# Kernel optimization log

Hardware: AMD Instinct MI355X
Metric: run time of the kernel (lower is better)

Reference implementation:

```python
import jax, jax.numpy as jnp
import numpy as np

B, N, C, H = 32, 577, 768, 12  # seq len = num_patches + 1 (cls token)
HD = C // H
SCALE = HD ** -0.5


def setup_inputs() -> dict:
    key = jax.random.key(0)
    k1, k2, k3, k4, k5 = jax.random.split(key, 5)
    x = jax.random.normal(k1, (B, N, C), dtype=jnp.float32)
    qkv_w = jax.random.normal(k2, (3 * C, C), dtype=jnp.float32) * (C ** -0.5)
    proj_w = jax.random.normal(k3, (C, C), dtype=jnp.float32) * (C ** -0.5)
    proj_b = jax.random.normal(k4, (C,), dtype=jnp.float32) * 0.02
    # learned additive distance-bias mask (nn.Parameter in the original)
    attn_mask = jax.random.normal(k5, (H, N, N), dtype=jnp.float32) * 0.02
    return {"x": x, "qkv_w": qkv_w, "proj_w": proj_w, "proj_b": proj_b,
            "attn_mask": attn_mask}


def reference(x, qkv_w, proj_w, proj_b, attn_mask):
    b, n, c = x.shape
    # fused QKV projection (no bias, qkv_bias=False)
    qkv = (x @ qkv_w.T).reshape(b, n, 3, H, HD)
    qkv = jnp.transpose(qkv, (2, 0, 3, 1, 4))  # [3, B, H, N, HD]
    q, k, v = qkv[0], qkv[1], qkv[2]
    # scaled dot-product scores + learned additive mask (broadcast over batch)
    attn = jnp.einsum('bhnd,bhmd->bhnm', q, k) * SCALE + attn_mask
    attn = jax.nn.softmax(attn, axis=-1)
    out = jnp.einsum('bhnm,bhmd->bhnd', attn, v)
    out = jnp.transpose(out, (0, 2, 1, 3)).reshape(b, n, c)
    return out @ proj_w.T + proj_b
```

## Files before the change

kernel.cpp:

```cpp
#include <hip/hip_runtime.h>
#include <stdint.h>
#include <stddef.h>

#define B_SZ 32
#define NQ 577
#define CDIM 768
#define NH 12
#define HDIM 64
#define MROWS (B_SZ * NQ)
#define KDIM CDIM
#define NKT (KDIM / 64)
#define VT_STRIDE 640
#define MK_STRIDE 640
#define SCALE_F 0.125f

typedef __bf16 bf16x8 __attribute__((ext_vector_type(8)));
typedef float f32x4 __attribute__((ext_vector_type(4)));
typedef unsigned short u16x8 __attribute__((ext_vector_type(8)));
typedef unsigned short u16x4 __attribute__((ext_vector_type(4)));

__device__ __forceinline__ unsigned short f2bf(float f) {
    unsigned int u = __builtin_bit_cast(unsigned int, f);
    return (unsigned short)((u + 0x7fffu + ((u >> 16) & 1u)) >> 16);
}
__device__ __forceinline__ float bf2f(unsigned short u) {
    unsigned int v = ((unsigned int)u) << 16;
    return __builtin_bit_cast(float, v);
}

__device__ __forceinline__ f32x4 mfma16(bf16x8 a, bf16x8 b, f32x4 c) {
    return __builtin_amdgcn_mfma_f32_16x16x32_bf16(a, b, c, 0, 0, 0);
}

__device__ __forceinline__ void gll16(const void* g, void* l) {
    __builtin_amdgcn_global_load_lds(
        (const __attribute__((address_space(1))) void*)g,
        (__attribute__((address_space(3))) void*)l, 16, 0, 0);
}

__global__ __launch_bounds__(256) void cvt_bf16(
    const float* __restrict__ src, unsigned short* __restrict__ dst, int n8)
{
    int i = blockIdx.x * blockDim.x + threadIdx.x;
    int stride = gridDim.x * blockDim.x;
    for (; i < n8; i += stride) {
        const float* p = src + (size_t)i * 8;
        f32x4 v0 = *(const f32x4*)p;
        f32x4 v1 = *(const f32x4*)(p + 4);
        u16x8 u;
        u[0] = f2bf(v0[0]); u[1] = f2bf(v0[1]); u[2] = f2bf(v0[2]); u[3] = f2bf(v0[3]);
        u[4] = f2bf(v1[0]); u[5] = f2bf(v1[1]); u[6] = f2bf(v1[2]); u[7] = f2bf(v1[3]);
        *(u16x8*)(dst + (size_t)i * 8) = u;
    }
}

__global__ __launch_bounds__(256) void cvt_mask(
    const float* __restrict__ src, unsigned short* __restrict__ dst)
{
    const int CH = MK_STRIDE / 8;
    int i = blockIdx.x * blockDim.x + threadIdx.x;
    int total = NH * NQ * CH;
    if (i >= total) return;
    int row = i / CH, c8 = (i % CH) * 8;
    const float* s = src + (size_t)row * NQ;
    u16x8 u;
#pragma unroll
    for (int j = 0; j < 8; ++j) {
        int c = c8 + j;
        u[j] = (c < NQ) ? f2bf(s[c]) : (unsigned short)0;
    }
    *(u16x8*)(dst + (size_t)row * MK_STRIDE + c8) = u;
}


#define STAGE_HT8(SC, A_PTR, B_PTR)                                                \
    { const int _t = (SC) >> 2, _p = (SC) & 3;                                     \
      if (_t < NKT) {                                                              \
        const int _kh = _p >> 1;                                                   \
        unsigned short* _dst = (_p & 1) ? &Bl[_t & 1][_kh][0] : &Al[_t & 1][_kh][0];\
        const unsigned short* _sb = (_p & 1) ? (B_PTR) : (A_PTR);                  \
        const int _rb = ((_p & 1) ? nt : mt) * 256;                                \
        const int _k = _t * 64 + _kh * 32;                                         \
        const int _c0 = tid, _c1 = tid + 512;                                      \
        const int _g0 = _c0 ^ ((_c0 >> 3) & 7), _g1 = _c1 ^ ((_c1 >> 3) & 7);      \
        int _r0 = _rb + (_g0 >> 2), _r1 = _rb + (_g1 >> 2);                        \
        if (!(_p & 1)) {                                                           \
            if (_r0 >= MROWS) _r0 = MROWS - 1;                                     \
            if (_r1 >= MROWS) _r1 = MROWS - 1;                                     \
        }                                                                          \
        gll16(_sb + (size_t)_r0 * KDIM + _k + (_g0 & 3) * 8, _dst + _c0 * 8);      \
        gll16(_sb + (size_t)_r1 * KDIM + _k + (_g1 & 3) * 8, _dst + _c1 * 8);      \
      } else {                                                                     \
        gll16(A_PTR, &Scr[tid * 8]);                                               \
        gll16(A_PTR, &Scr[(tid + 512) * 8]);                                       \
      } }

#define GEMM8_MAINLOOP(A_PTR, B_PTR)                                               \
    const int tid = threadIdx.x;                                                   \
    const int wid = tid >> 6, lane = tid & 63;                                     \
    const int lo = lane & 15, hi = lane >> 4;                                      \
    const int wr = wid >> 2, wcN = wid & 3;                                        \
    f32x4 acc[8][4];                                                               \
    _Pragma("unroll") for (int i = 0; i < 8; ++i)                                  \
        _Pragma("unroll") for (int j = 0; j < 4; ++j)                              \
            acc[i][j] = (f32x4){0.f, 0.f, 0.f, 0.f};                               \
    const int xsw = ((4 * lo + hi) ^ ((lo >> 1) & 7)) * 16;                        \
    _Pragma("unroll") for (int ps = 0; ps < 7; ++ps) { STAGE_HT8(ps, A_PTR, B_PTR) } \
    int sc = 7;                                                                    \
    asm volatile("s_waitcnt vmcnt(6)" ::: "memory");                               \
    __builtin_amdgcn_s_barrier();                                                  \
    for (int t = 0; t < NKT; ++t) {                                                \
        const int db = t & 1;                                                      \
        const char* a0p = (const char*)&Al[db][0][0] + xsw;                        \
        const char* a1p = (const char*)&Al[db][1][0] + xsw;                        \
        const char* b0p = (const char*)&Bl[db][0][0] + xsw;                        \
        const char* b1p = (const char*)&Bl[db][1][0] + xsw;                        \
        bf16x8 a[8], bx[2], by[2];                                                 \
              \
        _Pragma("unroll") for (int mi = 0; mi < 8; ++mi)                           \
            a[mi] = *(const bf16x8*)(a0p + (wr * 8 + mi) * 1024);                  \
        bx[0] = *(const bf16x8*)(b0p + (wcN * 4 + 0) * 1024);                      \
        bx[1] = *(const bf16x8*)(b0p + (wcN * 4 + 1) * 1024);                      \
        asm volatile("" ::: "memory");                                             \
        STAGE_HT8(sc, A_PTR, B_PTR) ++sc;                                          \
        __builtin_amdgcn_s_barrier();                                              \
        __builtin_amdgcn_s_setprio(1);                                             \
        _Pragma("unroll") for (int mi = 0; mi < 8; ++mi) {                         \
            acc[mi][0] = mfma16(a[mi], bx[0], acc[mi][0]);                         \
            acc[mi][1] = mfma16(a[mi], bx[1], acc[mi][1]);                         \
        }                                                                          \
        __builtin_amdgcn_s_setprio(0);                                             \
        __builtin_amdgcn_s_barrier();                                              \
                               \
        by[0] = *(const bf16x8*)(b0p + (wcN * 4 + 2) * 1024);                      \
        by[1] = *(const bf16x8*)(b0p + (wcN * 4 + 3) * 1024);                      \
        asm volatile("" ::: "memory");                                             \
        STAGE_HT8(sc, A_PTR, B_PTR) ++sc;                                          \
        __builtin_amdgcn_s_barrier();                                              \
        __builtin_amdgcn_s_setprio(1);                                             \
        _Pragma("unroll") for (int mi = 0; mi < 8; ++mi) {                         \
            acc[mi][2] = mfma16(a[mi], by[0], acc[mi][2]);                         \
            acc[mi][3] = mfma16(a[mi], by[1], acc[mi][3]);                         \
        }                                                                          \
        __builtin_amdgcn_s_setprio(0);                                             \
        __builtin_amdgcn_s_barrier();                                              \
                    \
        _Pragma("unroll") for (int mi = 0; mi < 8; ++mi)                           \
            a[mi] = *(const bf16x8*)(a1p + (wr * 8 + mi) * 1024);                  \
        bx[0] = *(const bf16x8*)(b1p + (wcN * 4 + 0) * 1024);                      \
        bx[1] = *(const bf16x8*)(b1p + (wcN * 4 + 1) * 1024);                      \
        asm volatile("" ::: "memory");                                             \
        STAGE_HT8(sc, A_PTR, B_PTR) ++sc;                                          \
        __builtin_amdgcn_s_barrier();                                              \
        __builtin_amdgcn_s_setprio(1);                                             \
        _Pragma("unroll") for (int mi = 0; mi < 8; ++mi) {                         \
            acc[mi][0] = mfma16(a[mi], bx[0], acc[mi][0]);                         \
            acc[mi][1] = mfma16(a[mi], bx[1], acc[mi][1]);                         \
        }                                                                          \
        __builtin_amdgcn_s_setprio(0);                                             \
        __builtin_amdgcn_s_barrier();                                              \
               \
        by[0] = *(const bf16x8*)(b1p + (wcN * 4 + 2) * 1024);                      \
        by[1] = *(const bf16x8*)(b1p + (wcN * 4 + 3) * 1024);                      \
        asm volatile("" ::: "memory");                                             \
        STAGE_HT8(sc, A_PTR, B_PTR) ++sc;                                          \
        asm volatile("s_waitcnt vmcnt(6)" ::: "memory");                           \
        __builtin_amdgcn_s_barrier();                                              \
        __builtin_amdgcn_s_setprio(1);                                             \
        _Pragma("unroll") for (int mi = 0; mi < 8; ++mi) {                         \
            acc[mi][2] = mfma16(a[mi], by[0], acc[mi][2]);                         \
            acc[mi][3] = mfma16(a[mi], by[1], acc[mi][3]);                         \
        }                                                                          \
        __builtin_amdgcn_s_setprio(0);                                             \
        __builtin_amdgcn_s_barrier();                                              \
    }                                                                              \
    asm volatile("s_waitcnt vmcnt(0)" ::: "memory");

__global__ __launch_bounds__(512, 2) void qkv_gemm(
    const unsigned short* __restrict__ A,
    const unsigned short* __restrict__ Bm,
    unsigned short* __restrict__ qb,
    unsigned short* __restrict__ kb,
    unsigned short* __restrict__ vtb)
{
    __shared__ __align__(16) unsigned short Al[2][2][256 * 32];
    __shared__ __align__(16) unsigned short Bl[2][2][256 * 32];
    __shared__ __align__(16) unsigned short Scr[512 * 16];
    const int NTL = 9;
    const int xcd = blockIdx.x & 7, off = blockIdx.x >> 3;
    const int wgid = (xcd < 1 ? xcd * 83 : 83 + (xcd - 1) * 82) + off;
    const int nt = wgid % NTL, mt = wgid / NTL;

    GEMM8_MAINLOOP(A, Bm)

    const int cbase = nt * 256 + wcN * 64;
    const int s = cbase / CDIM;
    const int h = (cbase % CDIM) / HDIM;
#pragma unroll
    for (int mi = 0; mi < 8; ++mi) {
#pragma unroll
        for (int r = 0; r < 4; ++r) {
            int m = mt * 256 + wr * 128 + mi * 16 + 4 * hi + r;
            if (m >= MROWS) continue;
            int b = m / NQ, n = m % NQ;
            size_t bh = (size_t)(b * NH + h);
#pragma unroll
            for (int nj = 0; nj < 4; ++nj) {
                int d = nj * 16 + lo;
                unsigned short bv = f2bf(acc[mi][nj][r]);
                if (s == 0)      qb[(bh * NQ + n) * HDIM + d] = bv;
                else if (s == 1) kb[(bh * NQ + n) * HDIM + d] = bv;
                else             vtb[(bh * HDIM + d) * VT_STRIDE + n] = bv;
            }
        }
    }
}

__global__ __launch_bounds__(512, 2) void proj_gemm(
    const unsigned short* __restrict__ A,
    const unsigned short* __restrict__ Bm,
    const float* __restrict__ bias,
    float* __restrict__ out)
{
    __shared__ __align__(16) unsigned short Al[2][2][256 * 32];
    __shared__ __align__(16) unsigned short Bl[2][2][256 * 32];
    __shared__ __align__(16) unsigned short Scr[512 * 16];
    const int NTL = 3;
    const int xcd = blockIdx.x & 7, off = blockIdx.x >> 3;
    const int wgid = (xcd < 3 ? xcd * 28 : 84 + (xcd - 3) * 27) + off;
    const int nt = wgid % NTL, mt = wgid / NTL;

    GEMM8_MAINLOOP(A, Bm)

    const int cb = nt * 256 + wcN * 64;
    float bv[4];
#pragma unroll
    for (int nj = 0; nj < 4; ++nj) bv[nj] = bias[cb + nj * 16 + lo];
#pragma unroll
    for (int mi = 0; mi < 8; ++mi) {
#pragma unroll
        for (int r = 0; r < 4; ++r) {
            int m = mt * 256 + wr * 128 + mi * 16 + 4 * hi + r;
            if (m >= MROWS) continue;
#pragma unroll
            for (int nj = 0; nj < 4; ++nj)
                out[(size_t)m * CDIM + cb + nj * 16 + lo] = acc[mi][nj][r] + bv[nj];
        }
    }
}

#define STAGE(SEL, KV)                                                        \
    {                                                                         \
        int kr0 = (KV) + srow;      if (kr0 > NQ - 1) kr0 = NQ - 1;           \
        int kr1 = (KV) + srow + 32; if (kr1 > NQ - 1) kr1 = NQ - 1;           \
        gll16(kp + (size_t)kr0 * HDIM + scol, &Ks[SEL][0] + tid * 8);         \
        gll16(kp + (size_t)kr1 * HDIM + scol, &Ks[SEL][2048] + tid * 8);      \
        gll16(vp + (size_t)srow * VT_STRIDE + (KV) + scol, &Vs[SEL][0] + tid * 8); \
        gll16(vp + (size_t)(srow + 32) * VT_STRIDE + (KV) + scol, &Vs[SEL][2048] + tid * 8); \
    }

#define LOADM(MW, KV)                                                         \
    _Pragma("unroll") for (int nj = 0; nj < 4; ++nj)                          \
        MW[nj] = *(const u16x4*)(mrow + (KV) + 16 * nj + 4 * hi);

#define ATTN_COMPUTE(CB, KV)                                                  \
    {                                                                         \
        const int kv0 = (KV);                                                 \
        bf16x8 af0[4], af1[4], bv0[4], bv1[4];                                \
        _Pragma("unroll") for (int nj = 0; nj < 4; ++nj) {                    \
            int kr = 16 * nj + lo;                                            \
            int sw = (kr & 7) << 4;                                           \
            const unsigned short* rowp = &Ks[CB][kr * 64];                    \
            af0[nj] = *(const bf16x8*)(rowp + ((( 0 + 16 * hi) ^ sw) >> 1));  \
            af1[nj] = *(const bf16x8*)(rowp + (((64 + 16 * hi) ^ sw) >> 1));  \
        }                                                                     \
        _Pragma("unroll") for (int dj = 0; dj < 4; ++dj) {                    \
            int dr = 16 * dj + lo;                                            \
            int sw = (dr & 7) << 4;                                           \
            const unsigned short* rowp = &Vs[CB][dr * 64];                    \
            bv0[dj] = *(const bf16x8*)(rowp + ((( 0 + 16 * hi) ^ sw) >> 1));  \
            bv1[dj] = *(const bf16x8*)(rowp + (((64 + 16 * hi) ^ sw) >> 1));  \
        }                                                                     \
        __builtin_amdgcn_s_setprio(1);                                        \
        f32x4 S[4];                                                           \
        _Pragma("unroll") for (int nj = 0; nj < 4; ++nj) {                    \
            f32x4 sv = (f32x4){0.f, 0.f, 0.f, 0.f};                           \
            sv = mfma16(af0[nj], bq0, sv);                                    \
            sv = mfma16(af1[nj], bq1, sv);                                    \
            S[nj] = sv;                                                       \
        }                                                                     \
        __builtin_amdgcn_s_setprio(0);                                        \
        float p[16];                                                          \
        _Pragma("unroll") for (int nj = 0; nj < 4; ++nj)                      \
            _Pragma("unroll") for (int r = 0; r < 4; ++r)                     \
                p[nj * 4 + r] = S[nj][r] * SCALE_F + bf2f(mw[nj][r]);         \
        if (kv0 + 64 > NQ) {                                                  \
            const int rem = NQ - kv0;                                         \
            _Pragma("unroll") for (int nj = 0; nj < 4; ++nj)                  \
                _Pragma("unroll") for (int r = 0; r < 4; ++r)                 \
                    if (16 * nj + 4 * hi + r >= rem) p[nj * 4 + r] = -1e30f;  \
        }                                                                     \
        float m01 = fmaxf(p[0], p[1]),  m23 = fmaxf(p[2], p[3]);              \
        float m45 = fmaxf(p[4], p[5]),  m67 = fmaxf(p[6], p[7]);              \
        float m89 = fmaxf(p[8], p[9]),  mab = fmaxf(p[10], p[11]);            \
        float mcd = fmaxf(p[12], p[13]), mef = fmaxf(p[14], p[15]);           \
        float pmax = fmaxf(fmaxf(fmaxf(m01, m23), fmaxf(m45, m67)),           \
                           fmaxf(fmaxf(m89, mab), fmaxf(mcd, mef)));          \
        pmax = fmaxf(pmax, __shfl_xor(pmax, 16));                             \
        pmax = fmaxf(pmax, __shfl_xor(pmax, 32));                             \
        bool grow = pmax > m_run + 8.f;                                       \
        float mnew = grow ? pmax : m_run;                                     \
        float corr = __expf(m_run - mnew);                                    \
        m_run = mnew;                                                         \
        if (__any((int)grow)) {                                               \
            float c0 = __shfl(corr, 4 * hi + 0);                              \
            float c1 = __shfl(corr, 4 * hi + 1);                              \
            float c2 = __shfl(corr, 4 * hi + 2);                              \
            float c3 = __shfl(corr, 4 * hi + 3);                              \
            _Pragma("unroll") for (int dj = 0; dj < 4; ++dj) {                \
                accO[dj][0] *= c0; accO[dj][1] *= c1;                         \
                accO[dj][2] *= c2; accO[dj][3] *= c3;                         \
            }                                                                 \
        }                                                                     \
        _Pragma("unroll") for (int i = 0; i < 16; ++i)                        \
            p[i] = __expf(p[i] - mnew);                                       \
        float ps = (((p[0]+p[1])+(p[2]+p[3])) + ((p[4]+p[5])+(p[6]+p[7])))    \
                 + (((p[8]+p[9])+(p[10]+p[11])) + ((p[12]+p[13])+(p[14]+p[15])));\
        _Pragma("unroll") for (int nj = 0; nj < 4; ++nj) {                    \
            u16x4 w;                                                          \
            w[0] = f2bf(p[nj*4+0]); w[1] = f2bf(p[nj*4+1]);                   \
            w[2] = f2bf(p[nj*4+2]); w[3] = f2bf(p[nj*4+3]);                   \
            *(u16x4*)&P_lds[wv][lo][16 * nj + 4 * hi] = w;                    \
        }                                                                     \
        ps += __shfl_xor(ps, 16);                                             \
        ps += __shfl_xor(ps, 32);                                             \
        l_run = l_run * corr + ps;                                            \
        const bf16x8 pa0 = *(const bf16x8*)&P_lds[wv][lo][8 * hi];            \
        const bf16x8 pa1 = *(const bf16x8*)&P_lds[wv][lo][32 + 8 * hi];       \
        __builtin_amdgcn_s_setprio(1);                                        \
        _Pragma("unroll") for (int dj = 0; dj < 4; ++dj) {                    \
            accO[dj] = mfma16(pa0, bv0[dj], accO[dj]);                        \
            accO[dj] = mfma16(pa1, bv1[dj], accO[dj]);                        \
        }                                                                     \
        __builtin_amdgcn_s_setprio(0);                                        \
    }

__global__ __launch_bounds__(256) void attn_fused(
    const unsigned short* __restrict__ qb,
    const unsigned short* __restrict__ kb,
    const unsigned short* __restrict__ vtb,
    const unsigned short* __restrict__ maskb,
    unsigned short* __restrict__ ob)
{
    __shared__ unsigned short Ks[2][64 * 64];
    __shared__ unsigned short Vs[2][64 * 64];
    __shared__ unsigned short P_lds[4][16][68];
    const int tid = threadIdx.x;
    const int wv = tid >> 6;
    const int lane = tid & 63;
    const int lo = lane & 15, hi = lane >> 4;

    const int xcd = blockIdx.x & 7;
    const int idx = blockIdx.x >> 3;
    const int bh = xcd + 8 * (idx / 10);
    const int qblk = idx % 10;
    const int b = bh / NH, h = bh % NH;
    const int qt0 = qblk * 64;

    const unsigned short* qp = qb + (size_t)bh * NQ * HDIM;
    const unsigned short* kp = kb + (size_t)bh * NQ * HDIM;
    const unsigned short* vp = vtb + (size_t)bh * HDIM * VT_STRIDE;

    const int srow = tid >> 3;
    const int scol = ((((tid & 7) << 4) ^ ((srow & 7) << 4)) >> 1);

    int qr = qt0 + 16 * wv + lo; if (qr > NQ - 1) qr = NQ - 1;
    const unsigned short* mrow = maskb + ((size_t)h * NQ + qr) * MK_STRIDE;
    const bf16x8 bq0 = *(const bf16x8*)(qp + (size_t)qr * HDIM + 8 * hi);
    const bf16x8 bq1 = *(const bf16x8*)(qp + (size_t)qr * HDIM + 32 + 8 * hi);

    float m_run = -1e30f, l_run = 0.f;
    f32x4 accO[4];
#pragma unroll
    for (int dj = 0; dj < 4; ++dj) accO[dj] = (f32x4){0.f, 0.f, 0.f, 0.f};

    u16x4 mw[4];
    STAGE(0, 0)
    for (int t = 0; t < 9; ++t) {
        const int kv0 = t * 64;
        LOADM(mw, kv0)
        asm volatile("" ::: "memory");
        STAGE((t + 1) & 1, kv0 + 64)
        asm volatile("s_waitcnt vmcnt(8)" ::: "memory");
        __builtin_amdgcn_s_barrier();
        asm volatile("" ::: "memory");
        ATTN_COMPUTE(t & 1, kv0)
        asm volatile("" ::: "memory");
        __builtin_amdgcn_s_barrier();
    }
    LOADM(mw, 576)
    asm volatile("s_waitcnt vmcnt(4)" ::: "memory");
    __builtin_amdgcn_s_barrier();
    asm volatile("" ::: "memory");
    ATTN_COMPUTE(1, 576)

    float linv[4];
#pragma unroll
    for (int r = 0; r < 4; ++r) linv[r] = 1.0f / __shfl(l_run, 4 * hi + r);
#pragma unroll
    for (int r = 0; r < 4; ++r) {
        int row = qt0 + 16 * wv + 4 * hi + r;
        if (row >= NQ) continue;
        size_t base = ((size_t)b * NQ + row) * CDIM + h * HDIM;
#pragma unroll
        for (int dj = 0; dj < 4; ++dj)
            ob[base + dj * 16 + lo] = f2bf(accO[dj][r] * linv[r]);
    }
}

extern "C" void kernel_launch(void* const* d_in, const int* in_sizes, int n_in,
                              void* d_out, int out_size, void* d_ws, size_t ws_size,
                              hipStream_t stream) {
    (void)in_sizes; (void)n_in; (void)out_size; (void)ws_size;
    const float* x      = (const float*)d_in[0];
    const float* qkv_w  = (const float*)d_in[1];
    const float* proj_w = (const float*)d_in[2];
    const float* proj_b = (const float*)d_in[3];
    const float* mask   = (const float*)d_in[4];
    float* out = (float*)d_out;

    const size_t x_elems  = (size_t)MROWS * CDIM;
    const size_t w_elems  = (size_t)3 * CDIM * CDIM;
    const size_t pw_elems = (size_t)CDIM * CDIM;
    const size_t mk_elems = (size_t)NH * NQ * MK_STRIDE;
    const size_t qk_elems = (size_t)B_SZ * NH * NQ * HDIM;
    const size_t vt_elems = (size_t)B_SZ * NH * HDIM * VT_STRIDE;

    unsigned short* xb    = (unsigned short*)d_ws;
    unsigned short* wb    = xb + x_elems;
    unsigned short* pwb   = wb + w_elems;
    unsigned short* mkb   = pwb + pw_elems;
    unsigned short* vtbuf = mkb + mk_elems;
    unsigned short* qbuf  = vtbuf + vt_elems;
    unsigned short* kbuf  = qbuf + qk_elems;
    unsigned short* aobuf = xb;

    cvt_bf16<<<1024, 256, 0, stream>>>(x, xb, (int)(x_elems / 8));
    cvt_bf16<<<256, 256, 0, stream>>>(qkv_w, wb, (int)(w_elems / 8));
    cvt_bf16<<<128, 256, 0, stream>>>(proj_w, pwb, (int)(pw_elems / 8));
    cvt_mask<<<(NH * NQ * (MK_STRIDE / 8) + 255) / 256, 256, 0, stream>>>(mask, mkb);
    qkv_gemm<<<73 * 9, 512, 0, stream>>>(xb, wb, qbuf, kbuf, vtbuf);
    attn_fused<<<12 * 32 * 10, 256, 0, stream>>>(qbuf, kbuf, vtbuf, mkb, aobuf);
    proj_gemm<<<73 * 3, 512, 0, stream>>>(aobuf, pwb, proj_b, out);
}
```

Measured before the change: 311.6 us.

## Replace QKV GEMM with simpler 128x128 tile kernel using 256 threads

The QKV projection moves from the heavily pipelined 256x256-tile, 512-thread kernel to a simpler 128x128-tile, 256-thread kernel. It uses double-buffered direct-to-LDS loads over 32-wide K steps, with its own XCD-aware block mapping over 2610 blocks. The aim is more blocks and better wave balance across CUs for this shape. In exchange it gives up the deeper software pipeline and the swizzled LDS layout, which may cost data reuse and add LDS bank conflicts.

```diff
diff --git a/kernel.cpp b/kernel.cpp
--- a/kernel.cpp
+++ b/kernel.cpp
@@ -72,6 +72,90 @@
     *(u16x8*)(dst + (size_t)row * MK_STRIDE + c8) = u;
 }
 
+#define GEMM_MAINLOOP(A_PTR, B_PTR, MCLAMP)                                        \
+    const int tid = threadIdx.x;                                                   \
+    const int wv = tid >> 6, lane = tid & 63;                                      \
+    const int lo = lane & 15, hi = lane >> 4;                                      \
+    const int wr = wv >> 1, wc = wv & 1;                                           \
+    f32x4 acc[4][4];                                                               \
+    _Pragma("unroll") for (int i = 0; i < 4; ++i)                                  \
+        _Pragma("unroll") for (int j = 0; j < 4; ++j)                              \
+            acc[i][j] = (f32x4){0.f, 0.f, 0.f, 0.f};                               \
+    const int c0 = wv * 128 + lane;                                                \
+    const int c1 = c0 + 64;                                                        \
+    const int rA0 = c0 >> 2, kA0 = (c0 & 3) * 8;                                   \
+    const int rA1 = c1 >> 2, kA1 = (c1 & 3) * 8;                                   \
+    int gra0 = mt * 128 + rA0; if (MCLAMP && gra0 >= MROWS) gra0 = MROWS - 1;      \
+    int gra1 = mt * 128 + rA1; if (MCLAMP && gra1 >= MROWS) gra1 = MROWS - 1;      \
+    const int grb0 = nt * 128 + rA0, grb1 = nt * 128 + rA1;                        \
+    gll16(A_PTR + (size_t)gra0 * KDIM + kA0, &As[0][c0 * 8]);                      \
+    gll16(A_PTR + (size_t)gra1 * KDIM + kA1, &As[0][c1 * 8]);                      \
+    gll16(B_PTR + (size_t)grb0 * KDIM + kA0, &Bs[0][c0 * 8]);                      \
+    gll16(B_PTR + (size_t)grb1 * KDIM + kA1, &Bs[0][c1 * 8]);                      \
+    for (int ks = 0; ks < KDIM / 32; ++ks) {                                       \
+        const int cur = ks & 1, nxt = cur ^ 1;                                     \
+        if (ks + 1 < KDIM / 32) {                                                  \
+            const int k0n = (ks + 1) * 32;                                         \
+            gll16(A_PTR + (size_t)gra0 * KDIM + k0n + kA0, &As[nxt][c0 * 8]);      \
+            gll16(A_PTR + (size_t)gra1 * KDIM + k0n + kA1, &As[nxt][c1 * 8]);      \
+            gll16(B_PTR + (size_t)grb0 * KDIM + k0n + kA0, &Bs[nxt][c0 * 8]);      \
+            gll16(B_PTR + (size_t)grb1 * KDIM + k0n + kA1, &Bs[nxt][c1 * 8]);      \
+            asm volatile("s_waitcnt vmcnt(4)" ::: "memory");                       \
+        } else {                                                                   \
+            asm volatile("s_waitcnt vmcnt(0)" ::: "memory");                       \
+        }                                                                          \
+        __builtin_amdgcn_s_barrier();                                              \
+        bf16x8 af[4], bfr[4];                                                      \
+        _Pragma("unroll") for (int mi = 0; mi < 4; ++mi)                           \
+            af[mi] = *(const bf16x8*)(&As[cur][(wr * 64 + mi * 16 + lo) * 32 + hi * 8]); \
+        _Pragma("unroll") for (int nj = 0; nj < 4; ++nj)                           \
+            bfr[nj] = *(const bf16x8*)(&Bs[cur][(wc * 64 + nj * 16 + lo) * 32 + hi * 8]); \
+        __builtin_amdgcn_s_setprio(1);                                             \
+        _Pragma("unroll") for (int mi = 0; mi < 4; ++mi)                           \
+            _Pragma("unroll") for (int nj = 0; nj < 4; ++nj)                       \
+                acc[mi][nj] = mfma16(af[mi], bfr[nj], acc[mi][nj]);                \
+        __builtin_amdgcn_s_setprio(0);                                             \
+        __builtin_amdgcn_s_barrier();                                              \
+    }
+
+__global__ __launch_bounds__(256) void qkv_gemm(
+    const unsigned short* __restrict__ A,
+    const unsigned short* __restrict__ Bm,
+    unsigned short* __restrict__ qb,
+    unsigned short* __restrict__ kb,
+    unsigned short* __restrict__ vtb)
+{
+    __shared__ unsigned short As[2][128 * 32];
+    __shared__ unsigned short Bs[2][128 * 32];
+    const int NT = 18;
+    const int q8 = 326, r8 = 2;
+    const int xcd = blockIdx.x & 7, off = blockIdx.x >> 3;
+    const int wgid = (xcd < r8 ? xcd * (q8 + 1) : r8 * (q8 + 1) + (xcd - r8) * q8) + off;
+    int nt = wgid % NT, mt = wgid / NT;
+
+    GEMM_MAINLOOP(A, Bm, 1)
+
+    const int s = nt / 6;
+    const int h = (nt % 6) * 2 + wc;
+#pragma unroll
+    for (int mi = 0; mi < 4; ++mi) {
+#pragma unroll
+        for (int r = 0; r < 4; ++r) {
+            int m = mt * 128 + wr * 64 + mi * 16 + hi * 4 + r;
+            if (m >= MROWS) continue;
+            int b = m / NQ, n = m % NQ;
+            size_t bh = (size_t)(b * NH + h);
+#pragma unroll
+            for (int nj = 0; nj < 4; ++nj) {
+                int d = nj * 16 + lo;
+                unsigned short bv = f2bf(acc[mi][nj][r]);
+                if (s == 0)      qb[(bh * NQ + n) * HDIM + d] = bv;
+                else if (s == 1) kb[(bh * NQ + n) * HDIM + d] = bv;
+                else             vtb[(bh * HDIM + d) * VT_STRIDE + n] = bv;
+            }
+        }
+    }
+}
 
 #define STAGE_HT8(SC, A_PTR, B_PTR)                                                \
     { const int _t = (SC) >> 2, _p = (SC) & 3;                                     \
@@ -116,7 +200,6 @@
         const char* b0p = (const char*)&Bl[db][0][0] + xsw;                        \
         const char* b1p = (const char*)&Bl[db][1][0] + xsw;                        \
         bf16x8 a[8], bx[2], by[2];                                                 \
-              \
         _Pragma("unroll") for (int mi = 0; mi < 8; ++mi)                           \
             a[mi] = *(const bf16x8*)(a0p + (wr * 8 + mi) * 1024);                  \
         bx[0] = *(const bf16x8*)(b0p + (wcN * 4 + 0) * 1024);                      \
@@ -131,7 +214,6 @@
         }                                                                          \
         __builtin_amdgcn_s_setprio(0);                                             \
         __builtin_amdgcn_s_barrier();                                              \
-                               \
         by[0] = *(const bf16x8*)(b0p + (wcN * 4 + 2) * 1024);                      \
         by[1] = *(const bf16x8*)(b0p + (wcN * 4 + 3) * 1024);                      \
         asm volatile("" ::: "memory");                                             \
@@ -144,7 +226,6 @@
         }                                                                          \
         __builtin_amdgcn_s_setprio(0);                                             \
         __builtin_amdgcn_s_barrier();                                              \
-                    \
         _Pragma("unroll") for (int mi = 0; mi < 8; ++mi)                           \
             a[mi] = *(const bf16x8*)(a1p + (wr * 8 + mi) * 1024);                  \
         bx[0] = *(const bf16x8*)(b1p + (wcN * 4 + 0) * 1024);                      \
@@ -159,7 +240,6 @@
         }                                                                          \
         __builtin_amdgcn_s_setprio(0);                                             \
         __builtin_amdgcn_s_barrier();                                              \
-               \
         by[0] = *(const bf16x8*)(b1p + (wcN * 4 + 2) * 1024);                      \
         by[1] = *(const bf16x8*)(b1p + (wcN * 4 + 3) * 1024);                      \
         asm volatile("" ::: "memory");                                             \
@@ -175,46 +255,6 @@
         __builtin_amdgcn_s_barrier();                                              \
     }                                                                              \
     asm volatile("s_waitcnt vmcnt(0)" ::: "memory");
-
-__global__ __launch_bounds__(512, 2) void qkv_gemm(
-    const unsigned short* __restrict__ A,
-    const unsigned short* __restrict__ Bm,
-    unsigned short* __restrict__ qb,
-    unsigned short* __restrict__ kb,
-    unsigned short* __restrict__ vtb)
-{
-    __shared__ __align__(16) unsigned short Al[2][2][256 * 32];
-    __shared__ __align__(16) unsigned short Bl[2][2][256 * 32];
-    __shared__ __align__(16) unsigned short Scr[512 * 16];
-    const int NTL = 9;
-    const int xcd = blockIdx.x & 7, off = blockIdx.x >> 3;
-    const int wgid = (xcd < 1 ? xcd * 83 : 83 + (xcd - 1) * 82) + off;
-    const int nt = wgid % NTL, mt = wgid / NTL;
-
-    GEMM8_MAINLOOP(A, Bm)
-
-    const int cbase = nt * 256 + wcN * 64;
-    const int s = cbase / CDIM;
-    const int h = (cbase % CDIM) / HDIM;
-#pragma unroll
-    for (int mi = 0; mi < 8; ++mi) {
-#pragma unroll
-        for (int r = 0; r < 4; ++r) {
-            int m = mt * 256 + wr * 128 + mi * 16 + 4 * hi + r;
-            if (m >= MROWS) continue;
-            int b = m / NQ, n = m % NQ;
-            size_t bh = (size_t)(b * NH + h);
-#pragma unroll
-            for (int nj = 0; nj < 4; ++nj) {
-                int d = nj * 16 + lo;
-                unsigned short bv = f2bf(acc[mi][nj][r]);
-                if (s == 0)      qb[(bh * NQ + n) * HDIM + d] = bv;
-                else if (s == 1) kb[(bh * NQ + n) * HDIM + d] = bv;
-                else             vtb[(bh * HDIM + d) * VT_STRIDE + n] = bv;
-            }
-        }
-    }
-}
 
 __global__ __launch_bounds__(512, 2) void proj_gemm(
     const unsigned short* __restrict__ A,
@@ -449,7 +489,7 @@
     cvt_bf16<<<256, 256, 0, stream>>>(qkv_w, wb, (int)(w_elems / 8));
     cvt_bf16<<<128, 256, 0, stream>>>(proj_w, pwb, (int)(pw_elems / 8));
     cvt_mask<<<(NH * NQ * (MK_STRIDE / 8) + 255) / 256, 256, 0, stream>>>(mask, mkb);
-    qkv_gemm<<<73 * 9, 512, 0, stream>>>(xb, wb, qbuf, kbuf, vtbuf);
+    qkv_gemm<<<145 * 18, 256, 0, stream>>>(xb, wb, qbuf, kbuf, vtbuf);
     attn_fused<<<12 * 32 * 10, 256, 0, stream>>>(qbuf, kbuf, vtbuf, mkb, aobuf);
     proj_gemm<<<73 * 3, 512, 0, stream>>>(aobuf, pwb, proj_b, out);
 }
```

After: 305.5 us. 1.02x faster.

## Replace 256x256 QKV GEMM with single-wave 64x64 tile kernel

Applied to the files above, without the earlier changes.

Replaces the large 512-thread, 256x256-tile QKV GEMM with a 64-thread kernel that computes a 64x64 output tile per workgroup, double-buffering 32-wide K slices in LDS. Each tile maps exactly to one of q/k/v and one head, and the grid grows to 10404 workgroups to spread better across CUs and avoid the wave quantization of the 657 large tiles. The trade-off is much less data reuse per tile, so global and L2 traffic for A and B rises, and there are more, smaller workgroups.

```diff
diff --git a/kernel.cpp b/kernel.cpp
--- a/kernel.cpp
+++ b/kernel.cpp
@@ -72,6 +72,109 @@
     *(u16x8*)(dst + (size_t)row * MK_STRIDE + c8) = u;
 }
 
+__global__ __launch_bounds__(64) void qkv_gemm(
+    const unsigned short* __restrict__ A,
+    const unsigned short* __restrict__ Bm,
+    unsigned short* __restrict__ qb,
+    unsigned short* __restrict__ kb,
+    unsigned short* __restrict__ vtb)
+{
+    __shared__ unsigned short As[2][64 * 32];
+    __shared__ unsigned short Bs[2][64 * 32];
+    const int t = threadIdx.x;
+    const int lo = t & 15, hi = t >> 4;
+
+    const int xcd = blockIdx.x & 7, off = blockIdx.x >> 3;
+    const int wgid = (xcd < 4 ? xcd * 1301 : 4 * 1301 + (xcd - 4) * 1300) + off;
+    const int NT = 36;
+    const int nt = wgid % NT, mt = wgid / NT;
+
+    const unsigned short* asrc[4];
+    const unsigned short* bsrc[4];
+#pragma unroll
+    for (int j = 0; j < 4; ++j) {
+        int c = 64 * j + t;
+        int s = c ^ ((c >> 3) & 7);
+        int ar = mt * 64 + (s >> 2); if (ar >= MROWS) ar = MROWS - 1;
+        int br = nt * 64 + (s >> 2);
+        asrc[j] = A + (size_t)ar * KDIM + (s & 3) * 8;
+        bsrc[j] = Bm + (size_t)br * KDIM + (s & 3) * 8;
+    }
+    int aoff[4], boff[4];
+#pragma unroll
+    for (int mi = 0; mi < 4; ++mi) {
+        int g = (mi * 16 + lo) * 4 + hi;
+        aoff[mi] = (g ^ ((g >> 3) & 7)) * 16;
+    }
+#pragma unroll
+    for (int nj = 0; nj < 4; ++nj) {
+        int g = (nj * 16 + lo) * 4 + hi;
+        boff[nj] = (g ^ ((g >> 3) & 7)) * 16;
+    }
+
+    f32x4 acc[4][4];
+#pragma unroll
+    for (int i = 0; i < 4; ++i)
+#pragma unroll
+        for (int j = 0; j < 4; ++j) acc[i][j] = (f32x4){0.f, 0.f, 0.f, 0.f};
+
+#pragma unroll
+    for (int j = 0; j < 4; ++j) {
+        gll16(asrc[j], &As[0][(64 * j + t) * 8]);
+        gll16(bsrc[j], &Bs[0][(64 * j + t) * 8]);
+    }
+
+    for (int ks = 0; ks < 24; ++ks) {
+        const int cur = ks & 1, nxt = cur ^ 1;
+        if (ks < 23) {
+            const int k0 = (ks + 1) * 32;
+#pragma unroll
+            for (int j = 0; j < 4; ++j) {
+                gll16(asrc[j] + k0, &As[nxt][(64 * j + t) * 8]);
+                gll16(bsrc[j] + k0, &Bs[nxt][(64 * j + t) * 8]);
+            }
+            asm volatile("s_waitcnt vmcnt(8)" ::: "memory");
+        } else {
+            asm volatile("s_waitcnt vmcnt(0)" ::: "memory");
+        }
+        bf16x8 af[4], bfr[4];
+#pragma unroll
+        for (int mi = 0; mi < 4; ++mi)
+            af[mi] = *(const bf16x8*)((const char*)&As[cur][0] + aoff[mi]);
+#pragma unroll
+        for (int nj = 0; nj < 4; ++nj)
+            bfr[nj] = *(const bf16x8*)((const char*)&Bs[cur][0] + boff[nj]);
+        __builtin_amdgcn_s_setprio(1);
+#pragma unroll
+        for (int mi = 0; mi < 4; ++mi)
+#pragma unroll
+            for (int nj = 0; nj < 4; ++nj)
+                acc[mi][nj] = mfma16(af[mi], bfr[nj], acc[mi][nj]);
+        __builtin_amdgcn_s_setprio(0);
+        asm volatile("" ::: "memory");
+    }
+
+    const int s = nt / 12;
+    const int h = nt % 12;
+#pragma unroll
+    for (int mi = 0; mi < 4; ++mi) {
+#pragma unroll
+        for (int r = 0; r < 4; ++r) {
+            int m = mt * 64 + mi * 16 + 4 * hi + r;
+            if (m >= MROWS) continue;
+            int b = m / NQ, n = m % NQ;
+            size_t bh = (size_t)(b * NH + h);
+#pragma unroll
+            for (int nj = 0; nj < 4; ++nj) {
+                int d = nj * 16 + lo;
+                unsigned short bv = f2bf(acc[mi][nj][r]);
+                if (s == 0)      qb[(bh * NQ + n) * HDIM + d] = bv;
+                else if (s == 1) kb[(bh * NQ + n) * HDIM + d] = bv;
+                else             vtb[(bh * HDIM + d) * VT_STRIDE + n] = bv;
+            }
+        }
+    }
+}
 
 #define STAGE_HT8(SC, A_PTR, B_PTR)                                                \
     { const int _t = (SC) >> 2, _p = (SC) & 3;                                     \
@@ -116,7 +219,6 @@
         const char* b0p = (const char*)&Bl[db][0][0] + xsw;                        \
         const char* b1p = (const char*)&Bl[db][1][0] + xsw;                        \
         bf16x8 a[8], bx[2], by[2];                                                 \
-              \
         _Pragma("unroll") for (int mi = 0; mi < 8; ++mi)                           \
             a[mi] = *(const bf16x8*)(a0p + (wr * 8 + mi) * 1024);                  \
         bx[0] = *(const bf16x8*)(b0p + (wcN * 4 + 0) * 1024);                      \
@@ -131,7 +233,6 @@
         }                                                                          \
         __builtin_amdgcn_s_setprio(0);                                             \
         __builtin_amdgcn_s_barrier();                                              \
-                               \
         by[0] = *(const bf16x8*)(b0p + (wcN * 4 + 2) * 1024);                      \
         by[1] = *(const bf16x8*)(b0p + (wcN * 4 + 3) * 1024);                      \
         asm volatile("" ::: "memory");                                             \
@@ -144,7 +245,6 @@
         }                                                                          \
         __builtin_amdgcn_s_setprio(0);                                             \
         __builtin_amdgcn_s_barrier();                                              \
-                    \
         _Pragma("unroll") for (int mi = 0; mi < 8; ++mi)                           \
             a[mi] = *(const bf16x8*)(a1p + (wr * 8 + mi) * 1024);                  \
         bx[0] = *(const bf16x8*)(b1p + (wcN * 4 + 0) * 1024);                      \
@@ -159,7 +259,6 @@
         }                                                                          \
         __builtin_amdgcn_s_setprio(0);                                             \
         __builtin_amdgcn_s_barrier();                                              \
-               \
         by[0] = *(const bf16x8*)(b1p + (wcN * 4 + 2) * 1024);                      \
         by[1] = *(const bf16x8*)(b1p + (wcN * 4 + 3) * 1024);                      \
         asm volatile("" ::: "memory");                                             \
@@ -175,46 +274,6 @@
         __builtin_amdgcn_s_barrier();                                              \
     }                                                                              \
     asm volatile("s_waitcnt vmcnt(0)" ::: "memory");
-
-__global__ __launch_bounds__(512, 2) void qkv_gemm(
-    const unsigned short* __restrict__ A,
-    const unsigned short* __restrict__ Bm,
-    unsigned short* __restrict__ qb,
-    unsigned short* __restrict__ kb,
-    unsigned short* __restrict__ vtb)
-{
-    __shared__ __align__(16) unsigned short Al[2][2][256 * 32];
-    __shared__ __align__(16) unsigned short Bl[2][2][256 * 32];
-    __shared__ __align__(16) unsigned short Scr[512 * 16];
-    const int NTL = 9;
-    const int xcd = blockIdx.x & 7, off = blockIdx.x >> 3;
-    const int wgid = (xcd < 1 ? xcd * 83 : 83 + (xcd - 1) * 82) + off;
-    const int nt = wgid % NTL, mt = wgid / NTL;
-
-    GEMM8_MAINLOOP(A, Bm)
-
-    const int cbase = nt * 256 + wcN * 64;
-    const int s = cbase / CDIM;
-    const int h = (cbase % CDIM) / HDIM;
-#pragma unroll
-    for (int mi = 0; mi < 8; ++mi) {
-#pragma unroll
-        for (int r = 0; r < 4; ++r) {
-            int m = mt * 256 + wr * 128 + mi * 16 + 4 * hi + r;
-            if (m >= MROWS) continue;
-            int b = m / NQ, n = m % NQ;
-            size_t bh = (size_t)(b * NH + h);
-#pragma unroll
-            for (int nj = 0; nj < 4; ++nj) {
-                int d = nj * 16 + lo;
-                unsigned short bv = f2bf(acc[mi][nj][r]);
-                if (s == 0)      qb[(bh * NQ + n) * HDIM + d] = bv;
-                else if (s == 1) kb[(bh * NQ + n) * HDIM + d] = bv;
-                else             vtb[(bh * HDIM + d) * VT_STRIDE + n] = bv;
-            }
-        }
-    }
-}
 
 __global__ __launch_bounds__(512, 2) void proj_gemm(
     const unsigned short* __restrict__ A,
@@ -449,7 +508,7 @@
     cvt_bf16<<<256, 256, 0, stream>>>(qkv_w, wb, (int)(w_elems / 8));
     cvt_bf16<<<128, 256, 0, stream>>>(proj_w, pwb, (int)(pw_elems / 8));
     cvt_mask<<<(NH * NQ * (MK_STRIDE / 8) + 255) / 256, 256, 0, stream>>>(mask, mkb);
-    qkv_gemm<<<73 * 9, 512, 0, stream>>>(xb, wb, qbuf, kbuf, vtbuf);
+    qkv_gemm<<<289 * 36, 64, 0, stream>>>(xb, wb, qbuf, kbuf, vtbuf);
     attn_fused<<<12 * 32 * 10, 256, 0, stream>>>(qbuf, kbuf, vtbuf, mkb, aobuf);
     proj_gemm<<<73 * 3, 512, 0, stream>>>(aobuf, pwb, proj_b, out);
 }
```

New measurement: 345.6 us. 1.11x slower.

## Replace QKV GEMM with 128x128-tile, 256-thread kernel using triple-buffered loads

Applied to the files above, without the earlier changes.

The QKV projection GEMM moves from the shared 256x256-tile, 512-thread main loop to a dedicated kernel with 128x128 tiles, 4 waves and a 3-stage global-to-LDS pipeline over K in steps of 32. The grid grows from 657 to 2610 workgroups, which should improve load balance and wave-quantization across CUs and lower LDS pressure, with the XCD-aware workgroup remapping kept. In exchange each tile has less operand reuse, the LDS reads are unswizzled and may hit bank conflicts, and there is one barrier pair per small K step.

```diff
diff --git a/kernel.cpp b/kernel.cpp
--- a/kernel.cpp
+++ b/kernel.cpp
@@ -72,6 +72,102 @@
     *(u16x8*)(dst + (size_t)row * MK_STRIDE + c8) = u;
 }
 
+__global__ __launch_bounds__(256) void qkv_gemm(
+    const unsigned short* __restrict__ A,
+    const unsigned short* __restrict__ Bm,
+    unsigned short* __restrict__ qb,
+    unsigned short* __restrict__ kb,
+    unsigned short* __restrict__ vtb)
+{
+    __shared__ unsigned short As[3][128 * 32];
+    __shared__ unsigned short Bs[3][128 * 32];
+    const int tid = threadIdx.x;
+    const int wv = tid >> 6, lane = tid & 63;
+    const int lo = lane & 15, hi = lane >> 4;
+    const int wr = wv >> 1, wc = wv & 1;
+
+    const int NT = 18;
+    const int q8 = 326, r8 = 2;
+    const int xcd = blockIdx.x & 7, off = blockIdx.x >> 3;
+    const int wgid = (xcd < r8 ? xcd * (q8 + 1) : r8 * (q8 + 1) + (xcd - r8) * q8) + off;
+    const int nt = wgid % NT, mt = wgid / NT;
+
+    f32x4 acc[4][4];
+#pragma unroll
+    for (int i = 0; i < 4; ++i)
+#pragma unroll
+        for (int j = 0; j < 4; ++j) acc[i][j] = (f32x4){0.f, 0.f, 0.f, 0.f};
+
+    const int c0 = wv * 128 + lane;
+    const int c1 = c0 + 64;
+    const int rA0 = c0 >> 2, kA0 = (c0 & 3) * 8;
+    const int rA1 = c1 >> 2, kA1 = (c1 & 3) * 8;
+    int gra0 = mt * 128 + rA0; if (gra0 >= MROWS) gra0 = MROWS - 1;
+    int gra1 = mt * 128 + rA1; if (gra1 >= MROWS) gra1 = MROWS - 1;
+    const int grb0 = nt * 128 + rA0, grb1 = nt * 128 + rA1;
+
+#define QKV_STG(BUF, KS)                                                      \
+    {                                                                         \
+        const int _k = (KS) * 32;                                             \
+        gll16(A  + (size_t)gra0 * KDIM + _k + kA0, &As[BUF][c0 * 8]);         \
+        gll16(A  + (size_t)gra1 * KDIM + _k + kA1, &As[BUF][c1 * 8]);         \
+        gll16(Bm + (size_t)grb0 * KDIM + _k + kA0, &Bs[BUF][c0 * 8]);         \
+        gll16(Bm + (size_t)grb1 * KDIM + _k + kA1, &Bs[BUF][c1 * 8]);         \
+    }
+
+    QKV_STG(0, 0)
+    QKV_STG(1, 1)
+
+    for (int ks = 0; ks < 24; ++ks) {
+        const int cur = ks % 3;
+        if (ks + 2 < 24) {
+            QKV_STG((ks + 2) % 3, ks + 2)
+            asm volatile("s_waitcnt vmcnt(8)" ::: "memory");
+        } else if (ks + 1 < 24) {
+            asm volatile("s_waitcnt vmcnt(4)" ::: "memory");
+        } else {
+            asm volatile("s_waitcnt vmcnt(0)" ::: "memory");
+        }
+        __builtin_amdgcn_s_barrier();
+        bf16x8 af[4], bfr[4];
+#pragma unroll
+        for (int mi = 0; mi < 4; ++mi)
+            af[mi] = *(const bf16x8*)(&As[cur][(wr * 64 + mi * 16 + lo) * 32 + hi * 8]);
+#pragma unroll
+        for (int nj = 0; nj < 4; ++nj)
+            bfr[nj] = *(const bf16x8*)(&Bs[cur][(wc * 64 + nj * 16 + lo) * 32 + hi * 8]);
+        __builtin_amdgcn_s_setprio(1);
+#pragma unroll
+        for (int mi = 0; mi < 4; ++mi)
+#pragma unroll
+            for (int nj = 0; nj < 4; ++nj)
+                acc[mi][nj] = mfma16(af[mi], bfr[nj], acc[mi][nj]);
+        __builtin_amdgcn_s_setprio(0);
+        __builtin_amdgcn_s_barrier();
+    }
+#undef QKV_STG
+
+    const int s = nt / 6;
+    const int h = (nt % 6) * 2 + wc;
+#pragma unroll
+    for (int mi = 0; mi < 4; ++mi) {
+#pragma unroll
+        for (int r = 0; r < 4; ++r) {
+            int m = mt * 128 + wr * 64 + mi * 16 + hi * 4 + r;
+            if (m >= MROWS) continue;
+            int b = m / NQ, n = m % NQ;
+            size_t bh = (size_t)(b * NH + h);
+#pragma unroll
+            for (int nj = 0; nj < 4; ++nj) {
+                int d = nj * 16 + lo;
+                unsigned short bv = f2bf(acc[mi][nj][r]);
+                if (s == 0)      qb[(bh * NQ + n) * HDIM + d] = bv;
+                else if (s == 1) kb[(bh * NQ + n) * HDIM + d] = bv;
+                else             vtb[(bh * HDIM + d) * VT_STRIDE + n] = bv;
+            }
+        }
+    }
+}
 
 #define STAGE_HT8(SC, A_PTR, B_PTR)                                                \
     { const int _t = (SC) >> 2, _p = (SC) & 3;                                     \
@@ -116,7 +212,6 @@
         const char* b0p = (const char*)&Bl[db][0][0] + xsw;                        \
         const char* b1p = (const char*)&Bl[db][1][0] + xsw;                        \
         bf16x8 a[8], bx[2], by[2];                                                 \
-              \
         _Pragma("unroll") for (int mi = 0; mi < 8; ++mi)                           \
             a[mi] = *(const bf16x8*)(a0p + (wr * 8 + mi) * 1024);                  \
         bx[0] = *(const bf16x8*)(b0p + (wcN * 4 + 0) * 1024);                      \
@@ -131,7 +226,6 @@
         }                                                                          \
         __builtin_amdgcn_s_setprio(0);                                             \
         __builtin_amdgcn_s_barrier();                                              \
-                               \
         by[0] = *(const bf16x8*)(b0p + (wcN * 4 + 2) * 1024);                      \
         by[1] = *(const bf16x8*)(b0p + (wcN * 4 + 3) * 1024);                      \
         asm volatile("" ::: "memory");                                             \
@@ -144,7 +238,6 @@
         }                                                                          \
         __builtin_amdgcn_s_setprio(0);                                             \
         __builtin_amdgcn_s_barrier();                                              \
-                    \
         _Pragma("unroll") for (int mi = 0; mi < 8; ++mi)                           \
             a[mi] = *(const bf16x8*)(a1p + (wr * 8 + mi) * 1024);                  \
         bx[0] = *(const bf16x8*)(b1p + (wcN * 4 + 0) * 1024);                      \
@@ -159,7 +252,6 @@
         }                                                                          \
         __builtin_amdgcn_s_setprio(0);                                             \
         __builtin_amdgcn_s_barrier();                                              \
-               \
         by[0] = *(const bf16x8*)(b1p + (wcN * 4 + 2) * 1024);                      \
         by[1] = *(const bf16x8*)(b1p + (wcN * 4 + 3) * 1024);                      \
         asm volatile("" ::: "memory");                                             \
@@ -175,46 +267,6 @@
         __builtin_amdgcn_s_barrier();                                              \
     }                                                                              \
     asm volatile("s_waitcnt vmcnt(0)" ::: "memory");
-
-__global__ __launch_bounds__(512, 2) void qkv_gemm(
-    const unsigned short* __restrict__ A,
-    const unsigned short* __restrict__ Bm,
-    unsigned short* __restrict__ qb,
-    unsigned short* __restrict__ kb,
-    unsigned short* __restrict__ vtb)
-{
-    __shared__ __align__(16) unsigned short Al[2][2][256 * 32];
-    __shared__ __align__(16) unsigned short Bl[2][2][256 * 32];
-    __shared__ __align__(16) unsigned short Scr[512 * 16];
-    const int NTL = 9;
-    const int xcd = blockIdx.x & 7, off = blockIdx.x >> 3;
-    const int wgid = (xcd < 1 ? xcd * 83 : 83 + (xcd - 1) * 82) + off;
-    const int nt = wgid % NTL, mt = wgid / NTL;
-
-    GEMM8_MAINLOOP(A, Bm)
-
-    const int cbase = nt * 256 + wcN * 64;
-    const int s = cbase / CDIM;
-    const int h = (cbase % CDIM) / HDIM;
-#pragma unroll
-    for (int mi = 0; mi < 8; ++mi) {
-#pragma unroll
-        for (int r = 0; r < 4; ++r) {
-            int m = mt * 256 + wr * 128 + mi * 16 + 4 * hi + r;
-            if (m >= MROWS) continue;
-            int b = m / NQ, n = m % NQ;
-            size_t bh = (size_t)(b * NH + h);
-#pragma unroll
-            for (int nj = 0; nj < 4; ++nj) {
-                int d = nj * 16 + lo;
-                unsigned short bv = f2bf(acc[mi][nj][r]);
-                if (s == 0)      qb[(bh * NQ + n) * HDIM + d] = bv;
-                else if (s == 1) kb[(bh * NQ + n) * HDIM + d] = bv;
-                else             vtb[(bh * HDIM + d) * VT_STRIDE + n] = bv;
-            }
-        }
-    }
-}
 
 __global__ __launch_bounds__(512, 2) void proj_gemm(
     const unsigned short* __restrict__ A,
@@ -449,7 +501,7 @@
     cvt_bf16<<<256, 256, 0, stream>>>(qkv_w, wb, (int)(w_elems / 8));
     cvt_bf16<<<128, 256, 0, stream>>>(proj_w, pwb, (int)(pw_elems / 8));
     cvt_mask<<<(NH * NQ * (MK_STRIDE / 8) + 255) / 256, 256, 0, stream>>>(mask, mkb);
-    qkv_gemm<<<73 * 9, 512, 0, stream>>>(xb, wb, qbuf, kbuf, vtbuf);
+    qkv_gemm<<<145 * 18, 256, 0, stream>>>(xb, wb, qbuf, kbuf, vtbuf);
     attn_fused<<<12 * 32 * 10, 256, 0, stream>>>(qbuf, kbuf, vtbuf, mkb, aobuf);
     proj_gemm<<<73 * 3, 512, 0, stream>>>(aobuf, pwb, proj_b, out);
 }
```

New measurement: 305.1 us, median of 2. 1.02x faster.
